# Kernel optimization log

Measured on AMD Instinct MI355X. Metric: run time of the kernel, lower is better.

Reference implementation:

```python
import jax, jax.numpy as jnp
import numpy as np

K = 8
N = 32768
L = 512  # latent_dim
SCALE = 1.0  # params in torch are tiny ((2u-1)/(K*out)); randn here, math identical


def _fkan(x, A, B):
    # x: [N, in]; A, B: [out, in, K]
    # y[b,o] = sum_{i,k} A[o,i,k]*sin(k*x[b,i]) + B[o,i,k]*cos(k*x[b,i])
    k = jnp.arange(K, dtype=x.dtype)            # [K]
    kx = x[..., None] * k                       # [N, in, K]
    return (jnp.einsum('bik,oik->bo', jnp.sin(kx), A)
            + jnp.einsum('bik,oik->bo', jnp.cos(kx), B))


def setup_inputs() -> dict:
    key = jax.random.key(0)
    ks = jax.random.split(key, 11)
    shapes = [(L, 1, K), (L, L, K), (L, L, K), (L, L, K), (1, L, K)]
    inp = {'x': jax.random.normal(ks[0], (N, 1), dtype=jnp.float32)}
    for li, shp in enumerate(shapes):
        # mimic torch init scale (2u-1)/(K*out)
        out = shp[0]
        inp[f'A{li}'] = (2.0 * jax.random.uniform(ks[1 + 2 * li], shp, dtype=jnp.float32) - 1.0) / (K * out)
        inp[f'B{li}'] = (2.0 * jax.random.uniform(ks[2 + 2 * li], shp, dtype=jnp.float32) - 1.0) / (K * out)
    return inp


def reference(x, A0, B0, A1, B1, A2, B2, A3, B3, A4, B4):
    for A, B in ((A0, B0), (A1, B1), (A2, B2), (A3, B3), (A4, B4)):
        x = _fkan(x, A, B)
    return x  # [N, 1]
```

## Files before the change

kernel.cpp:

```cpp
#include <hip/hip_runtime.h>
#include <hip/hip_bf16.h>
#include <math.h>

#define NB 32768
#define DIM 512
#define KF 8
#define FEAT 8192
#define BM 64
#define NSUP 64
#define NSTEP 128

typedef __attribute__((ext_vector_type(4))) int i32x4;
typedef unsigned short ushort_t;
typedef unsigned int uint_t;

#define WSCALE 520192.0f
#define OUT_SCALE (1.0f / (127.0f * 520192.0f))

static __device__ __forceinline__ ushort_t f2bf_s(float f) {
    return (ushort_t)((__float_as_uint(f) + 0x8000u) >> 16);
}
static __device__ __forceinline__ float bf2f(ushort_t u) {
    return __uint_as_float(((uint_t)u) << 16);
}

static __device__ __forceinline__ uint_t qb4(float a, float b, float c, float d) {
    const float MG = 12582912.0f;
    uint_t ua = __float_as_uint(a + MG);
    uint_t ub = __float_as_uint(b + MG);
    uint_t uc = __float_as_uint(c + MG);
    uint_t ud = __float_as_uint(d + MG);
    uint_t p1 = __builtin_amdgcn_perm(ub, ua, 0x0C0C0400u);
    uint_t p2 = __builtin_amdgcn_perm(ud, uc, 0x0C0C0400u);
    return __builtin_amdgcn_perm(p2, p1, 0x05040100u);
}

static __device__ __forceinline__ i32x4 feat_q16(float xv) {
    float s1, c1;
    __sincosf(xv, &s1, &c1);
    float S[KF], C[KF];
    S[0] = 0.f; C[0] = 127.f;
    S[1] = 127.f * s1; C[1] = 127.f * c1;
#pragma unroll
    for (int k = 2; k < KF; ++k) {
        S[k] = S[k - 1] * c1 + C[k - 1] * s1;
        C[k] = C[k - 1] * c1 - S[k - 1] * s1;
    }
    i32x4 r;
    r[0] = (int)qb4(S[0], S[1], S[2], S[3]);
    r[1] = (int)qb4(S[4], S[5], S[6], S[7]);
    r[2] = (int)qb4(C[0], C[1], C[2], C[3]);
    r[3] = (int)qb4(C[4], C[5], C[6], C[7]);
    return r;
}

static __device__ __forceinline__ int pk4w(const float* w) {
    int q[4];
#pragma unroll
    for (int j = 0; j < 4; ++j) {
        int v = __float2int_rn(w[j] * WSCALE);
        v = v > 127 ? 127 : (v < -127 ? -127 : v);
        q[j] = v & 255;
    }
    return (int)((uint_t)q[0] | ((uint_t)q[1] << 8) | ((uint_t)q[2] << 16) | ((uint_t)q[3] << 24));
}

__global__ void pack_w8(const float* __restrict__ A, const float* __restrict__ B,
                        i32x4* __restrict__ Wf) {
    int u = blockIdx.x * 256 + threadIdx.x;
    int lane = u & 63;
    int n = (u >> 6) & 3, wb = (u >> 8) & 7, t = u >> 11;
    int o = wb * 64 + n * 16 + (lane & 15);
    int i = t * 4 + (lane >> 4);
    const float* a = A + ((size_t)o * DIM + i) * KF;
    const float* b = B + ((size_t)o * DIM + i) * KF;
    i32x4 v;
    v[0] = pk4w(a);
    v[1] = pk4w(a + 4);
    v[2] = pk4w(b);
    v[3] = pk4w(b + 4);
    Wf[u] = v;
}

__global__ void layer0(const float* __restrict__ x, const float* __restrict__ A0,
                       const float* __restrict__ B0, ushort_t* __restrict__ Y) {
    int gid = blockIdx.x * 256 + threadIdx.x;
    int b = gid >> 9, o = gid & 511;
    float xv = x[b];
    float s1, c1;
    __sincosf(xv, &s1, &c1);
    const float* a = A0 + o * KF;
    const float* bb = B0 + o * KF;
    float acc = bb[0];
    float sk = 0.f, ck = 1.f;
#pragma unroll
    for (int k = 1; k < KF; ++k) {
        float sn = sk * c1 + ck * s1;
        float cn = ck * c1 - sk * s1;
        sk = sn; ck = cn;
        acc += a[k] * sk + bb[k] * ck;
    }
    Y[gid] = f2bf_s(acc);
}

__global__ __launch_bounds__(256, 2) void fkan_gemm(const ushort_t* __restrict__ X,
                                                    const i32x4* __restrict__ Wf,
                                                    ushort_t* __restrict__ Y) {
    __shared__ i32x4 ring[8][256];
    const int tid = threadIdx.x;
    const int lane = tid & 63, wave = tid >> 6;
    const int l15 = lane & 15, l4 = lane >> 4;
    const int bm0 = blockIdx.x * BM;

    const int bl = tid >> 2, ii = tid & 3;
    const ushort_t* xp = X + (size_t)(bm0 + bl) * DIM + ii;
    const int wunit = (bl >> 1) * 8 + (((ii * 2 + (bl & 1)) ^ ((bl >> 1) & 7)));

    int runit[4];
#pragma unroll
    for (int m = 0; m < 4; ++m) {
        int r = m * 16 + l15;
        runit[m] = (r >> 1) * 8 + (((l4 * 2 + (r & 1)) ^ ((r >> 1) & 7)));
    }

    const i32x4* bp = Wf + lane;
    int boff[8];
#pragma unroll
    for (int n = 0; n < 8; ++n)
        boff[n] = (2 * wave + (n >> 2)) * 256 + (n & 3) * 64;

    i32x4 acc[4][8];
#pragma unroll
    for (int m = 0; m < 4; ++m)
#pragma unroll
        for (int n = 0; n < 8; ++n) acc[m][n] = (i32x4)0;

#pragma unroll
    for (int t = 0; t < 4; ++t)
        ring[t][wunit] = feat_q16(bf2f(xp[t * 4]));
    i32x4 c[8];
#pragma unroll
    for (int n = 0; n < 8; ++n) c[n] = bp[boff[n]];
    float xvA = bf2f(xp[16]);
    float xvB = bf2f(xp[20]);
    asm volatile("s_waitcnt lgkmcnt(0)" ::: "memory");
    __builtin_amdgcn_s_barrier();

    for (int T = 0; T < NSUP; ++T) {
        const i32x4* rd0 = &ring[(2 * T) & 7][0];
        const i32x4* rd1 = &ring[(2 * T + 1) & 7][0];
        i32x4* wr0 = &ring[(2 * T + 4) & 7][0];
        i32x4* wr1 = &ring[(2 * T + 5) & 7][0];
        const size_t t0 = 2 * (size_t)T;
        const bool stg = (T + 2 < NSUP);

        i32x4 af0[4], af1[4];
#pragma unroll
        for (int m = 0; m < 4; ++m) af0[m] = rd0[runit[m]];
#pragma unroll
        for (int m = 0; m < 4; ++m) af1[m] = rd1[runit[m]];

        __builtin_amdgcn_s_setprio(1);
#pragma unroll
        for (int n = 0; n < 8; ++n) {
#pragma unroll
            for (int m = 0; m < 4; ++m)
                acc[m][n] = __builtin_amdgcn_mfma_i32_16x16x64_i8(af0[m], c[n], acc[m][n], 0, 0, 0);
            c[n] = bp[boff[n] + (t0 + 1) * 2048];
        }
        __builtin_amdgcn_s_setprio(0);
        if (stg)
            wr0[wunit] = feat_q16(xvA);

        __builtin_amdgcn_s_setprio(1);
        if (T + 1 < NSUP) {
#pragma unroll
            for (int n = 0; n < 8; ++n) {
#pragma unroll
                for (int m = 0; m < 4; ++m)
                    acc[m][n] = __builtin_amdgcn_mfma_i32_16x16x64_i8(af1[m], c[n], acc[m][n], 0, 0, 0);
                c[n] = bp[boff[n] + (t0 + 2) * 2048];
            }
        } else {
#pragma unroll
            for (int n = 0; n < 8; ++n)
#pragma unroll
                for (int m = 0; m < 4; ++m)
                    acc[m][n] = __builtin_amdgcn_mfma_i32_16x16x64_i8(af1[m], c[n], acc[m][n], 0, 0, 0);
        }
        __builtin_amdgcn_s_setprio(0);
        if (stg) {
            wr1[wunit] = feat_q16(xvB);
            if (T + 3 < NSUP) {
                xvA = bf2f(xp[(t0 + 6) * 4]);
                xvB = bf2f(xp[(t0 + 7) * 4]);
            }
        }

        if (T & 1) {
            asm volatile("s_waitcnt lgkmcnt(0)" ::: "memory");
            __builtin_amdgcn_s_barrier();
        }
    }

#pragma unroll
    for (int m = 0; m < 4; ++m)
#pragma unroll
        for (int n = 0; n < 8; ++n)
#pragma unroll
            for (int j = 0; j < 4; ++j) {
                int row = bm0 + m * 16 + l4 * 4 + j;
                int col = wave * 128 + n * 16 + l15;
                Y[(size_t)row * DIM + col] = f2bf_s((float)acc[m][n][j] * OUT_SCALE);
            }
}

__global__ void layer4(const ushort_t* __restrict__ X, const float* __restrict__ A4,
                       const float* __restrict__ B4, float* __restrict__ Y) {
    int wave = threadIdx.x >> 6, lane = threadIdx.x & 63;
    int b = blockIdx.x * 4 + wave;
    float acc = 0.f;
#pragma unroll
    for (int ii = 0; ii < 8; ++ii) {
        int i = lane + ii * 64;
        float xv = bf2f(X[(size_t)b * DIM + i]);
        float s1, c1;
        __sincosf(xv, &s1, &c1);
        const float* a = A4 + i * KF;
        const float* bb = B4 + i * KF;
        acc += bb[0];
        float sk = 0.f, ck = 1.f;
#pragma unroll
        for (int k = 1; k < KF; ++k) {
            float sn = sk * c1 + ck * s1;
            float cn = ck * c1 - sk * s1;
            sk = sn; ck = cn;
            acc += a[k] * sk + bb[k] * ck;
        }
    }
#pragma unroll
    for (int off = 32; off > 0; off >>= 1) acc += __shfl_down(acc, off, 64);
    if (lane == 0) Y[b] = acc;
}

extern "C" void kernel_launch(void* const* d_in, const int* in_sizes, int n_in,
                              void* d_out, int out_size, void* d_ws, size_t ws_size,
                              hipStream_t stream) {
    const float* x  = (const float*)d_in[0];
    const float* A0 = (const float*)d_in[1];
    const float* B0 = (const float*)d_in[2];
    const float* A1 = (const float*)d_in[3];
    const float* B1 = (const float*)d_in[4];
    const float* A2 = (const float*)d_in[5];
    const float* B2 = (const float*)d_in[6];
    const float* A3 = (const float*)d_in[7];
    const float* B3 = (const float*)d_in[8];
    const float* A4 = (const float*)d_in[9];
    const float* B4 = (const float*)d_in[10];
    float* out = (float*)d_out;

    char* ws = (char*)d_ws;
    const size_t actBytes = (size_t)NB * DIM * sizeof(ushort_t);
    const size_t wBytes = (size_t)DIM * FEAT;
    ushort_t* bufA = (ushort_t*)ws;
    ushort_t* bufB = (ushort_t*)(ws + actBytes);
    i32x4* W1 = (i32x4*)(ws + 2 * actBytes);
    i32x4* W2 = (i32x4*)(ws + 2 * actBytes + wBytes);
    i32x4* W3 = (i32x4*)(ws + 2 * actBytes + 2 * wBytes);

    pack_w8<<<DIM * FEAT / 16 / 256, 256, 0, stream>>>(A1, B1, W1);
    pack_w8<<<DIM * FEAT / 16 / 256, 256, 0, stream>>>(A2, B2, W2);
    pack_w8<<<DIM * FEAT / 16 / 256, 256, 0, stream>>>(A3, B3, W3);

    layer0<<<(NB * DIM) / 256, 256, 0, stream>>>(x, A0, B0, bufA);

    fkan_gemm<<<NB / BM, 256, 0, stream>>>(bufA, W1, bufB);
    fkan_gemm<<<NB / BM, 256, 0, stream>>>(bufB, W2, bufA);
    fkan_gemm<<<NB / BM, 256, 0, stream>>>(bufA, W3, bufB);

    layer4<<<NB / 4, 256, 0, stream>>>(bufB, A4, B4, out);
}
```

Measured before the change: 448.8 us.

## Switch int8 GEMM from 16x16x64 to 32x32x32 MFMA with repacked weights

Replaces the 16x16x64 int8 MFMA tiles with 32x32x32 int8 MFMA, so each wave holds 2x4 32x32 accumulators instead of 4x8 16x16. The weight pack kernel is rewritten to lay out B fragments for the new operand format, and LDS read indices and the output store mapping are changed to match. It also drops the s_setprio hints and uses byte-offset weight loads. The larger MFMA shape is meant to cut instruction-issue overhead and improve operand reuse per instruction, at the cost of a new fragment layout that must match exactly.

```diff
diff --git a/kernel.cpp b/kernel.cpp
--- a/kernel.cpp
+++ b/kernel.cpp
@@ -8,9 +8,9 @@
 #define FEAT 8192
 #define BM 64
 #define NSUP 64
-#define NSTEP 128
 
 typedef __attribute__((ext_vector_type(4))) int i32x4;
+typedef __attribute__((ext_vector_type(16))) int i32x16;
 typedef unsigned short ushort_t;
 typedef unsigned int uint_t;
 
@@ -65,13 +65,14 @@
     return (int)((uint_t)q[0] | ((uint_t)q[1] << 8) | ((uint_t)q[2] << 16) | ((uint_t)q[3] << 24));
 }
 
-__global__ void pack_w8(const float* __restrict__ A, const float* __restrict__ B,
-                        i32x4* __restrict__ Wf) {
+__global__ void pack_w32(const float* __restrict__ A, const float* __restrict__ B,
+                         i32x4* __restrict__ Wf) {
     int u = blockIdx.x * 256 + threadIdx.x;
     int lane = u & 63;
-    int n = (u >> 6) & 3, wb = (u >> 8) & 7, t = u >> 11;
-    int o = wb * 64 + n * 16 + (lane & 15);
-    int i = t * 4 + (lane >> 4);
+    int q = u >> 6;
+    int nt = q & 3, w = (q >> 2) & 3, kb = (q >> 4) & 1, t = q >> 5;
+    int o = w * 128 + nt * 32 + (lane & 31);
+    int i = t * 4 + kb * 2 + (lane >> 5);
     const float* a = A + ((size_t)o * DIM + i) * KF;
     const float* b = B + ((size_t)o * DIM + i) * KF;
     i32x4 v;
@@ -109,91 +110,89 @@
     __shared__ i32x4 ring[8][256];
     const int tid = threadIdx.x;
     const int lane = tid & 63, wave = tid >> 6;
-    const int l15 = lane & 15, l4 = lane >> 4;
     const int bm0 = blockIdx.x * BM;
 
     const int bl = tid >> 2, ii = tid & 3;
-    const ushort_t* xp = X + (size_t)(bm0 + bl) * DIM + ii;
+    const ushort_t* xq = X + (size_t)(bm0 + bl) * DIM + ii;
     const int wunit = (bl >> 1) * 8 + (((ii * 2 + (bl & 1)) ^ ((bl >> 1) & 7)));
 
     int runit[4];
 #pragma unroll
-    for (int m = 0; m < 4; ++m) {
-        int r = m * 16 + l15;
-        runit[m] = (r >> 1) * 8 + (((l4 * 2 + (r & 1)) ^ ((r >> 1) & 7)));
-    }
-
-    const i32x4* bp = Wf + lane;
-    int boff[8];
-#pragma unroll
-    for (int n = 0; n < 8; ++n)
-        boff[n] = (2 * wave + (n >> 2)) * 256 + (n & 3) * 64;
-
-    i32x4 acc[4][8];
-#pragma unroll
-    for (int m = 0; m < 4; ++m)
-#pragma unroll
-        for (int n = 0; n < 8; ++n) acc[m][n] = (i32x4)0;
+    for (int m = 0; m < 2; ++m)
+#pragma unroll
+        for (int kb = 0; kb < 2; ++kb) {
+            int r = m * 32 + (lane & 31);
+            int inp = kb * 2 + (lane >> 5);
+            runit[m * 2 + kb] = (r >> 1) * 8 + (((inp * 2 + (r & 1)) ^ ((r >> 1) & 7)));
+        }
+
+    const char* wb = (const char*)Wf;
+    uint_t voff = (uint_t)(wave * 4096 + lane * 16);
+
+    i32x16 acc[2][4];
+#pragma unroll
+    for (int m = 0; m < 2; ++m)
+#pragma unroll
+        for (int n = 0; n < 4; ++n) acc[m][n] = (i32x16)0;
 
 #pragma unroll
     for (int t = 0; t < 4; ++t)
-        ring[t][wunit] = feat_q16(bf2f(xp[t * 4]));
+        ring[t][wunit] = feat_q16(bf2f(xq[t * 4]));
     i32x4 c[8];
 #pragma unroll
-    for (int n = 0; n < 8; ++n) c[n] = bp[boff[n]];
-    float xvA = bf2f(xp[16]);
-    float xvB = bf2f(xp[20]);
+    for (int kb = 0; kb < 2; ++kb)
+#pragma unroll
+        for (int n = 0; n < 4; ++n)
+            c[kb * 4 + n] = *(const i32x4*)(wb + voff + kb * 16384 + n * 1024);
+    voff += 32768u;
+    float xvA = bf2f(xq[16]);
+    float xvB = bf2f(xq[20]);
     asm volatile("s_waitcnt lgkmcnt(0)" ::: "memory");
     __builtin_amdgcn_s_barrier();
+
+#define MSTEP(AF, RELOAD)                                                                  \
+    {                                                                                      \
+        _Pragma("unroll")                                                                  \
+        for (int kb = 0; kb < 2; ++kb) {                                                   \
+            _Pragma("unroll")                                                              \
+            for (int n = 0; n < 4; ++n) {                                                  \
+                const int j = kb * 4 + n;                                                  \
+                acc[0][n] = __builtin_amdgcn_mfma_i32_32x32x32_i8(AF[kb],     c[j], acc[0][n], 0, 0, 0); \
+                acc[1][n] = __builtin_amdgcn_mfma_i32_32x32x32_i8(AF[2 + kb], c[j], acc[1][n], 0, 0, 0); \
+                if (RELOAD) c[j] = *(const i32x4*)(wb + voff + kb * 16384 + n * 1024);     \
+            }                                                                              \
+        }                                                                                  \
+        if (RELOAD) voff += 32768u;                                                        \
+    }
 
     for (int T = 0; T < NSUP; ++T) {
         const i32x4* rd0 = &ring[(2 * T) & 7][0];
         const i32x4* rd1 = &ring[(2 * T + 1) & 7][0];
         i32x4* wr0 = &ring[(2 * T + 4) & 7][0];
         i32x4* wr1 = &ring[(2 * T + 5) & 7][0];
-        const size_t t0 = 2 * (size_t)T;
         const bool stg = (T + 2 < NSUP);
+        const bool last = (T + 1 == NSUP);
 
         i32x4 af0[4], af1[4];
 #pragma unroll
-        for (int m = 0; m < 4; ++m) af0[m] = rd0[runit[m]];
-#pragma unroll
-        for (int m = 0; m < 4; ++m) af1[m] = rd1[runit[m]];
-
-        __builtin_amdgcn_s_setprio(1);
-#pragma unroll
-        for (int n = 0; n < 8; ++n) {
-#pragma unroll
-            for (int m = 0; m < 4; ++m)
-                acc[m][n] = __builtin_amdgcn_mfma_i32_16x16x64_i8(af0[m], c[n], acc[m][n], 0, 0, 0);
-            c[n] = bp[boff[n] + (t0 + 1) * 2048];
-        }
-        __builtin_amdgcn_s_setprio(0);
+        for (int q = 0; q < 4; ++q) af0[q] = rd0[runit[q]];
+#pragma unroll
+        for (int q = 0; q < 4; ++q) af1[q] = rd1[runit[q]];
+
+        MSTEP(af0, 1)
         if (stg)
             wr0[wunit] = feat_q16(xvA);
 
-        __builtin_amdgcn_s_setprio(1);
-        if (T + 1 < NSUP) {
-#pragma unroll
-            for (int n = 0; n < 8; ++n) {
-#pragma unroll
-                for (int m = 0; m < 4; ++m)
-                    acc[m][n] = __builtin_amdgcn_mfma_i32_16x16x64_i8(af1[m], c[n], acc[m][n], 0, 0, 0);
-                c[n] = bp[boff[n] + (t0 + 2) * 2048];
-            }
+        if (!last) {
+            MSTEP(af1, 1)
         } else {
-#pragma unroll
-            for (int n = 0; n < 8; ++n)
-#pragma unroll
-                for (int m = 0; m < 4; ++m)
-                    acc[m][n] = __builtin_amdgcn_mfma_i32_16x16x64_i8(af1[m], c[n], acc[m][n], 0, 0, 0);
-        }
-        __builtin_amdgcn_s_setprio(0);
+            MSTEP(af1, 0)
+        }
         if (stg) {
             wr1[wunit] = feat_q16(xvB);
             if (T + 3 < NSUP) {
-                xvA = bf2f(xp[(t0 + 6) * 4]);
-                xvB = bf2f(xp[(t0 + 7) * 4]);
+                xvA = bf2f(xq[(2 * T + 6) * 4]);
+                xvB = bf2f(xq[(2 * T + 7) * 4]);
             }
         }
 
@@ -202,16 +201,17 @@
             __builtin_amdgcn_s_barrier();
         }
     }
-
-#pragma unroll
-    for (int m = 0; m < 4; ++m)
-#pragma unroll
-        for (int n = 0; n < 8; ++n)
-#pragma unroll
-            for (int j = 0; j < 4; ++j) {
-                int row = bm0 + m * 16 + l4 * 4 + j;
-                int col = wave * 128 + n * 16 + l15;
-                Y[(size_t)row * DIM + col] = f2bf_s((float)acc[m][n][j] * OUT_SCALE);
+#undef MSTEP
+
+#pragma unroll
+    for (int m = 0; m < 2; ++m)
+#pragma unroll
+        for (int n = 0; n < 4; ++n)
+#pragma unroll
+            for (int r = 0; r < 16; ++r) {
+                int row = bm0 + m * 32 + (r & 3) + 8 * (r >> 2) + 4 * (lane >> 5);
+                int col = wave * 128 + n * 32 + (lane & 31);
+                Y[(size_t)row * DIM + col] = f2bf_s((float)acc[m][n][r] * OUT_SCALE);
             }
 }
 
@@ -268,9 +268,9 @@
     i32x4* W2 = (i32x4*)(ws + 2 * actBytes + wBytes);
     i32x4* W3 = (i32x4*)(ws + 2 * actBytes + 2 * wBytes);
 
-    pack_w8<<<DIM * FEAT / 16 / 256, 256, 0, stream>>>(A1, B1, W1);
-    pack_w8<<<DIM * FEAT / 16 / 256, 256, 0, stream>>>(A2, B2, W2);
-    pack_w8<<<DIM * FEAT / 16 / 256, 256, 0, stream>>>(A3, B3, W3);
+    pack_w32<<<DIM * FEAT / 16 / 256, 256, 0, stream>>>(A1, B1, W1);
+    pack_w32<<<DIM * FEAT / 16 / 256, 256, 0, stream>>>(A2, B2, W2);
+    pack_w32<<<DIM * FEAT / 16 / 256, 256, 0, stream>>>(A3, B3, W3);
 
     layer0<<<(NB * DIM) / 256, 256, 0, stream>>>(x, A0, B0, bufA);
 
```

After: 521.3 us. +16.1%, slower.
